# Optimization experiments

Measured on AMD Instinct MI355X. Metric: run time of the kernel, lower is better.

The kernel has to match this reference:

```python
import jax, jax.numpy as jnp
import numpy as np

EMBEDDING_DIM = 64
N_EMBEDDINGS = 512


def setup_inputs() -> dict:
    key = jax.random.key(0)
    k1, k2 = jax.random.split(key)
    inputs = jax.random.normal(k1, (32, 64, 64, 64), dtype=jnp.float32)  # NCHW, C==embedding_dim
    weight = jax.random.normal(k2, (N_EMBEDDINGS, EMBEDDING_DIM), dtype=jnp.float32)
    return {"inputs": inputs, "weight": weight}


def reference(inputs, weight):
    # NCHW -> NHWC, flatten to [N, D]
    x = jnp.transpose(inputs, (0, 2, 3, 1))  # [B, H, W, D]
    in_shape = x.shape
    flat = x.reshape(-1, EMBEDDING_DIM)  # [N, D]

    distances = (
        jnp.sum(flat * flat, axis=1, keepdims=True)
        + jnp.sum(weight * weight, axis=1)
        - 2.0 * flat @ weight.T
    )
    idx = jnp.argmin(distances, axis=1)  # [N]

    # one-hot @ weight is just a gather
    quantized = weight[idx].reshape(in_shape)  # [B, H, W, D]

    # commitment loss: mse(stop_grad(quantized), x)
    e_latent_loss = jnp.mean(jnp.square(jax.lax.stop_gradient(quantized) - x))

    # straight-through estimator
    quantized = x + jax.lax.stop_gradient(quantized - x)

    return jnp.transpose(quantized, (0, 3, 1, 2)), e_latent_loss
```

## Files before the change

kernel.cpp:

```cpp
#include <hip/hip_runtime.h>
#include <math.h>

typedef short bf16x8 __attribute__((ext_vector_type(8)));
typedef float f32x4 __attribute__((ext_vector_type(4)));

#define VQ_D 64
#define VQ_K 512
#define VQ_NQ 131072
#define VQ_TOTAL 8388608
#define QB 128
#define NT 32
#define XPITCH 136

__device__ __forceinline__ ushort bf16_rne(float f) {
    uint u = __builtin_bit_cast(uint, f);
    u += 0x7fffu + ((u >> 16) & 1u);
    return (ushort)(u >> 16);
}
__device__ __forceinline__ float bf16_to_f(ushort h) {
    uint u = ((uint)h) << 16;
    return __builtin_bit_cast(float, u);
}

__global__ __launch_bounds__(64) void vq_prep(const float* __restrict__ w,
                                              ushort* __restrict__ wfrag,
                                              float* __restrict__ wn) {
    const int k = blockIdx.x * 64 + threadIdx.x;
    const float4* row = (const float4*)(w + k * VQ_D);
    const int t = k >> 4, col = k & 15;
    double sd = 0.0;
    for (int g = 0; g < 8; ++g) {
        float4 a = row[2 * g], b4 = row[2 * g + 1];
        float v[8] = {a.x, a.y, a.z, a.w, b4.x, b4.y, b4.z, b4.w};
        ushort hi[8], lo[8];
#pragma unroll
        for (int j = 0; j < 8; ++j) {
            sd = fma((double)v[j], (double)v[j], sd);
            hi[j] = bf16_rne(v[j]);
            lo[j] = bf16_rne(v[j] - bf16_to_f(hi[j]));
        }
        const int quad = g & 3, fh = g >> 2;
        const int lane = quad * 16 + col;
        bf16x8* basez = (bf16x8*)wfrag + t * 256 + lane;
        *(basez + (fh)*64)     = *(bf16x8*)hi;
        *(basez + (2 + fh)*64) = *(bf16x8*)lo;
    }
    wn[k] = (float)sd;
}

__global__ __launch_bounds__(256, 3) void vq_main(const float* __restrict__ in,
                                                  const float* __restrict__ w,
                                                  const ushort* __restrict__ wfrag,
                                                  const float* __restrict__ wng,
                                                  float* __restrict__ out) {
    __shared__ ushort x_lds[QB * XPITCH];
    __shared__ float wn_lds[VQ_K];
    __shared__ float xn_lds[2][QB];
    __shared__ float best_lds[QB], sec_lds[QB];
    __shared__ int   bi_lds[QB], si_lds[QB];

    const int tid  = threadIdx.x;
    const int lane = tid & 63;
    const int wid  = tid >> 6;
    const int col  = lane & 15;
    const int quad = lane >> 4;
    const int n0  = blockIdx.x * QB;
    const int b   = n0 >> 12;
    const int hw0 = n0 & 4095;
    const float* xg = in + (b << 18) + hw0;

    wn_lds[tid] = wng[tid];
    wn_lds[tid + 256] = wng[tid + 256];
    {
        const int q = tid & 127, gh = tid >> 7;
        const float* xq = xg + q;
        float xnp = 0.f;
#pragma unroll
        for (int i = 0; i < 4; ++i) {
            const int g = gh * 4 + i;
            float v[8];
            ushort hi[8], lo[8];
#pragma unroll
            for (int j = 0; j < 8; ++j) v[j] = xq[(g * 8 + j) << 12];
#pragma unroll
            for (int j = 0; j < 8; ++j) {
                xnp = fmaf(v[j], v[j], xnp);
                hi[j] = bf16_rne(v[j]);
                lo[j] = bf16_rne(v[j] - bf16_to_f(hi[j]));
            }
            *(bf16x8*)&x_lds[q * XPITCH + g * 8]      = *(bf16x8*)hi;
            *(bf16x8*)&x_lds[q * XPITCH + 64 + g * 8] = *(bf16x8*)lo;
        }
        xn_lds[gh][q] = xnp;
    }
    __syncthreads();

    const int arow0 = wid * 32 + col;
    bf16x8 ah0[2], ah1[2], al0[2], al1[2];
#pragma unroll
    for (int T = 0; T < 2; ++T) {
        const ushort* xr = x_lds + (arow0 + T * 16) * XPITCH;
        ah0[T] = *(const bf16x8*)(xr + quad * 8);
        ah1[T] = *(const bf16x8*)(xr + 32 + quad * 8);
        al0[T] = *(const bf16x8*)(xr + 64 + quad * 8);
        al1[T] = *(const bf16x8*)(xr + 96 + quad * 8);
    }

    float best[8], secnd[8];
    int bI[8], sI[8];
#pragma unroll
    for (int r = 0; r < 8; ++r) { best[r] = 3.4e38f; secnd[r] = 3.4e38f; bI[r] = 0; sI[r] = 0; }

    const bf16x8* wf = (const bf16x8*)wfrag + lane;
    bf16x8 bh0 = wf[0], bh1 = wf[64], bl0 = wf[128], bl1 = wf[192];

    for (int t = 0; t < NT; ++t) {
        bf16x8 nh0, nh1, nl0, nl1;
        if (t + 1 < NT) {
            const bf16x8* nx = wf + (t + 1) * 256;
            nh0 = nx[0]; nh1 = nx[64]; nl0 = nx[128]; nl1 = nx[192];
        }
        const float wnv = wn_lds[t * 16 + col];
#pragma unroll
        for (int T = 0; T < 2; ++T) {
            f32x4 accP = {0.f, 0.f, 0.f, 0.f}, accQ = {0.f, 0.f, 0.f, 0.f};
            accP = __builtin_amdgcn_mfma_f32_16x16x32_bf16(ah0[T], bh0, accP, 0, 0, 0);
            accP = __builtin_amdgcn_mfma_f32_16x16x32_bf16(ah1[T], bh1, accP, 0, 0, 0);
            accQ = __builtin_amdgcn_mfma_f32_16x16x32_bf16(ah0[T], bl0, accQ, 0, 0, 0);
            accQ = __builtin_amdgcn_mfma_f32_16x16x32_bf16(ah1[T], bl1, accQ, 0, 0, 0);
            accQ = __builtin_amdgcn_mfma_f32_16x16x32_bf16(al0[T], bh0, accQ, 0, 0, 0);
            accQ = __builtin_amdgcn_mfma_f32_16x16x32_bf16(al1[T], bh1, accQ, 0, 0, 0);
            const int kg = t * 16 + col;
#pragma unroll
            for (int j = 0; j < 4; ++j) {
                float dist = fmaf(-2.f, accP[j] + accQ[j], wnv);
                const int r = T * 4 + j;
                bool lt  = dist < best[r];
                bool lt2 = (!lt) && (dist < secnd[r]);
                secnd[r] = lt ? best[r] : (lt2 ? dist : secnd[r]);
                sI[r]    = lt ? bI[r]   : (lt2 ? kg   : sI[r]);
                best[r]  = lt ? dist    : best[r];
                bI[r]    = lt ? kg      : bI[r];
            }
        }
        bh0 = nh0; bh1 = nh1; bl0 = nl0; bl1 = nl1;
    }

#pragma unroll
    for (int off = 1; off < 16; off <<= 1) {
#pragma unroll
        for (int r = 0; r < 8; ++r) {
            float ob = __shfl_xor(best[r], off, 64);
            float os = __shfl_xor(secnd[r], off, 64);
            int   oi = __shfl_xor(bI[r], off, 64);
            int   oc = __shfl_xor(sI[r], off, 64);
            bool oWins = (ob < best[r]) || (ob == best[r] && oi < bI[r]);
            float nb  = oWins ? ob      : best[r];
            int   ni  = oWins ? oi      : bI[r];
            float c1  = oWins ? best[r] : ob;
            int   ci1 = oWins ? bI[r]   : oi;
            float c2  = oWins ? os      : secnd[r];
            int   ci2 = oWins ? oc      : sI[r];
            bool c1w = (c1 < c2) || (c1 == c2 && ci1 < ci2);
            secnd[r] = c1w ? c1 : c2;
            sI[r]    = c1w ? ci1 : ci2;
            best[r] = nb; bI[r] = ni;
        }
    }
    if (col == 0) {
#pragma unroll
        for (int r = 0; r < 8; ++r) {
            const int q = wid * 32 + (r >> 2) * 16 + quad * 4 + (r & 3);
            best_lds[q] = best[r]; sec_lds[q] = secnd[r];
            bi_lds[q] = bI[r];     si_lds[q] = sI[r];
        }
    }
    __syncthreads();

    if (tid < QB) {
        const int q = tid;
        float cb = best_lds[q], cs = sec_lds[q];
        int cbi = bi_lds[q], csi = si_lds[q];
        double chosen = (double)cb;
        if (cs - cb < 8e-3f) {
            const float* wb  = w + cbi * VQ_D;
            const float* ws2 = w + csi * VQ_D;
            const float* xqp = xg + q;
            double nb = 0.0, dotb = 0.0, ns = 0.0, dots = 0.0;
            for (int d = 0; d < VQ_D; ++d) {
                double xv = (double)xqp[d << 12];
                double wbv = (double)wb[d], wsv = (double)ws2[d];
                nb = fma(wbv, wbv, nb); dotb = fma(xv, wbv, dotb);
                ns = fma(wsv, wsv, ns); dots = fma(xv, wsv, dots);
            }
            double db = nb - 2.0 * dotb, ds = ns - 2.0 * dots;
            if (ds < db || (ds == db && csi < cbi)) { cbi = csi; chosen = ds; }
            else                                    { chosen = db; }
        }
        bi_lds[q] = cbi;
        double lq = (double)(xn_lds[0][q] + xn_lds[1][q]) + chosen;
#pragma unroll
        for (int off = 32; off > 0; off >>= 1)
            lq += __shfl_down(lq, off, 64);
        if ((tid & 63) == 0)
            atomicAdd(out + VQ_TOTAL, (float)(lq * (1.0 / (double)VQ_TOTAL)));
    }
    __syncthreads();

    {
        const int q = tid & 127, half = tid >> 7;
        const float4* wrow = (const float4*)(w + bi_lds[q] * VQ_D) + half * 8;
        float* op = out + (b << 18) + hw0 + q;
#pragma unroll
        for (int u = 0; u < 8; ++u) {
            float4 v = wrow[u];
            const int d = half * 32 + 4 * u;
            op[(d + 0) << 12] = v.x;
            op[(d + 1) << 12] = v.y;
            op[(d + 2) << 12] = v.z;
            op[(d + 3) << 12] = v.w;
        }
    }
}

extern "C" void kernel_launch(void* const* d_in, const int* in_sizes, int n_in,
                              void* d_out, int out_size, void* d_ws, size_t ws_size,
                              hipStream_t stream) {
    const float* in = (const float*)d_in[0];
    const float* w  = (const float*)d_in[1];
    float* out = (float*)d_out;

    ushort* wfrag = (ushort*)d_ws;
    float*  wn    = (float*)((char*)d_ws + 131072);

    hipMemsetAsync(out + VQ_TOTAL, 0, sizeof(float), stream);
    vq_prep<<<8, 64, 0, stream>>>(w, wfrag, wn);
    vq_main<<<VQ_NQ / QB, 256, 0, stream>>>(in, w, wfrag, wn, out);
}
```

Measured before the change: 141.0 us.

## Double queries per block and pack codebook tile index into distance low bits

Each block now handles 256 queries instead of 128, so every wave runs four 16-row MFMA tiles per codebook fragment load and the weight-fragment traffic per query is halved. The x tile is staged into LDS in two passes to keep the LDS footprint unchanged. The top-2 tracking in the inner loop packs the tile index into the low 5 mantissa bits of the distance, replacing compare-and-select chains with fmin/fmax. The memset is folded into the prep kernel, which also drops its double-precision norm accumulation. Register pressure rises (occupancy hint lowered from 3 to 2), and the bit packing slightly perturbs the distances, which the existing fp64 near-tie recheck is meant to absorb.

```diff
diff --git a/kernel.cpp b/kernel.cpp
--- a/kernel.cpp
+++ b/kernel.cpp
@@ -8,7 +8,7 @@
 #define VQ_K 512
 #define VQ_NQ 131072
 #define VQ_TOTAL 8388608
-#define QB 128
+#define QB 256
 #define NT 32
 #define XPITCH 136
 
@@ -22,38 +22,40 @@
     return __builtin_bit_cast(float, u);
 }
 
-__global__ __launch_bounds__(64) void vq_prep(const float* __restrict__ w,
-                                              ushort* __restrict__ wfrag,
-                                              float* __restrict__ wn) {
-    const int k = blockIdx.x * 64 + threadIdx.x;
+__global__ __launch_bounds__(128) void vq_prep(const float* __restrict__ w,
+                                               ushort* __restrict__ wfrag,
+                                               float* __restrict__ wn,
+                                               float* __restrict__ out) {
+    if (blockIdx.x == 0 && threadIdx.x == 0) out[VQ_TOTAL] = 0.f;
+    const int k = blockIdx.x * 128 + threadIdx.x;
     const float4* row = (const float4*)(w + k * VQ_D);
     const int t = k >> 4, col = k & 15;
-    double sd = 0.0;
+    float nrm = 0.f;
     for (int g = 0; g < 8; ++g) {
         float4 a = row[2 * g], b4 = row[2 * g + 1];
         float v[8] = {a.x, a.y, a.z, a.w, b4.x, b4.y, b4.z, b4.w};
         ushort hi[8], lo[8];
 #pragma unroll
         for (int j = 0; j < 8; ++j) {
-            sd = fma((double)v[j], (double)v[j], sd);
+            nrm = fmaf(v[j], v[j], nrm);
             hi[j] = bf16_rne(v[j]);
             lo[j] = bf16_rne(v[j] - bf16_to_f(hi[j]));
         }
         const int quad = g & 3, fh = g >> 2;
         const int lane = quad * 16 + col;
         bf16x8* basez = (bf16x8*)wfrag + t * 256 + lane;
-        *(basez + (fh)*64)     = *(bf16x8*)hi;
-        *(basez + (2 + fh)*64) = *(bf16x8*)lo;
-    }
-    wn[k] = (float)sd;
-}
-
-__global__ __launch_bounds__(256, 3) void vq_main(const float* __restrict__ in,
+        *(basez + fh * 64)       = *(bf16x8*)hi;
+        *(basez + (2 + fh) * 64) = *(bf16x8*)lo;
+    }
+    wn[k] = nrm;
+}
+
+__global__ __launch_bounds__(256, 2) void vq_main(const float* __restrict__ in,
                                                   const float* __restrict__ w,
                                                   const ushort* __restrict__ wfrag,
                                                   const float* __restrict__ wng,
                                                   float* __restrict__ out) {
-    __shared__ ushort x_lds[QB * XPITCH];
+    __shared__ ushort x_lds[128 * XPITCH];
     __shared__ float wn_lds[VQ_K];
     __shared__ float xn_lds[2][QB];
     __shared__ float best_lds[QB], sec_lds[QB];
@@ -69,47 +71,53 @@
     const int hw0 = n0 & 4095;
     const float* xg = in + (b << 18) + hw0;
 
-    wn_lds[tid] = wng[tid];
+    wn_lds[tid]       = wng[tid];
     wn_lds[tid + 256] = wng[tid + 256];
-    {
-        const int q = tid & 127, gh = tid >> 7;
-        const float* xq = xg + q;
-        float xnp = 0.f;
-#pragma unroll
-        for (int i = 0; i < 4; ++i) {
-            const int g = gh * 4 + i;
-            float v[8];
-            ushort hi[8], lo[8];
-#pragma unroll
-            for (int j = 0; j < 8; ++j) v[j] = xq[(g * 8 + j) << 12];
-#pragma unroll
-            for (int j = 0; j < 8; ++j) {
-                xnp = fmaf(v[j], v[j], xnp);
-                hi[j] = bf16_rne(v[j]);
-                lo[j] = bf16_rne(v[j] - bf16_to_f(hi[j]));
-            }
-            *(bf16x8*)&x_lds[q * XPITCH + g * 8]      = *(bf16x8*)hi;
-            *(bf16x8*)&x_lds[q * XPITCH + 64 + g * 8] = *(bf16x8*)lo;
-        }
-        xn_lds[gh][q] = xnp;
-    }
-    __syncthreads();
-
-    const int arow0 = wid * 32 + col;
-    bf16x8 ah0[2], ah1[2], al0[2], al1[2];
-#pragma unroll
-    for (int T = 0; T < 2; ++T) {
-        const ushort* xr = x_lds + (arow0 + T * 16) * XPITCH;
-        ah0[T] = *(const bf16x8*)(xr + quad * 8);
-        ah1[T] = *(const bf16x8*)(xr + 32 + quad * 8);
-        al0[T] = *(const bf16x8*)(xr + 64 + quad * 8);
-        al1[T] = *(const bf16x8*)(xr + 96 + quad * 8);
-    }
-
-    float best[8], secnd[8];
-    int bI[8], sI[8];
-#pragma unroll
-    for (int r = 0; r < 8; ++r) { best[r] = 3.4e38f; secnd[r] = 3.4e38f; bI[r] = 0; sI[r] = 0; }
+
+    bf16x8 ah0[4], ah1[4], al0[4], al1[4];
+    const int q_l = tid & 127, gh = tid >> 7;
+    const int arow_l = (wid & 1) * 64 + col;
+
+#pragma unroll
+    for (int p = 0; p < 2; ++p) {
+        {
+            const float* xq = xg + p * 128 + q_l;
+            float xnp = 0.f;
+#pragma unroll
+            for (int i = 0; i < 4; ++i) {
+                const int g = gh * 4 + i;
+                float v[8];
+                ushort hi[8], lo[8];
+#pragma unroll
+                for (int j = 0; j < 8; ++j) v[j] = xq[(g * 8 + j) << 12];
+#pragma unroll
+                for (int j = 0; j < 8; ++j) {
+                    xnp = fmaf(v[j], v[j], xnp);
+                    hi[j] = bf16_rne(v[j]);
+                    lo[j] = bf16_rne(v[j] - bf16_to_f(hi[j]));
+                }
+                *(bf16x8*)&x_lds[q_l * XPITCH + g * 8]      = *(bf16x8*)hi;
+                *(bf16x8*)&x_lds[q_l * XPITCH + 64 + g * 8] = *(bf16x8*)lo;
+            }
+            xn_lds[gh][p * 128 + q_l] = xnp;
+        }
+        __syncthreads();
+        if ((wid >> 1) == p) {
+#pragma unroll
+            for (int T = 0; T < 4; ++T) {
+                const ushort* xr = x_lds + (arow_l + T * 16) * XPITCH;
+                ah0[T] = *(const bf16x8*)(xr + quad * 8);
+                ah1[T] = *(const bf16x8*)(xr + 32 + quad * 8);
+                al0[T] = *(const bf16x8*)(xr + 64 + quad * 8);
+                al1[T] = *(const bf16x8*)(xr + 96 + quad * 8);
+            }
+        }
+        __syncthreads();
+    }
+
+    float best[16], secnd[16];
+#pragma unroll
+    for (int r = 0; r < 16; ++r) { best[r] = 3.0e38f; secnd[r] = 3.0e38f; }
 
     const bf16x8* wf = (const bf16x8*)wfrag + lane;
     bf16x8 bh0 = wf[0], bh1 = wf[64], bl0 = wf[128], bl1 = wf[192];
@@ -122,7 +130,7 @@
         }
         const float wnv = wn_lds[t * 16 + col];
 #pragma unroll
-        for (int T = 0; T < 2; ++T) {
+        for (int T = 0; T < 4; ++T) {
             f32x4 accP = {0.f, 0.f, 0.f, 0.f}, accQ = {0.f, 0.f, 0.f, 0.f};
             accP = __builtin_amdgcn_mfma_f32_16x16x32_bf16(ah0[T], bh0, accP, 0, 0, 0);
             accP = __builtin_amdgcn_mfma_f32_16x16x32_bf16(ah1[T], bh1, accP, 0, 0, 0);
@@ -130,54 +138,64 @@
             accQ = __builtin_amdgcn_mfma_f32_16x16x32_bf16(ah1[T], bl1, accQ, 0, 0, 0);
             accQ = __builtin_amdgcn_mfma_f32_16x16x32_bf16(al0[T], bh0, accQ, 0, 0, 0);
             accQ = __builtin_amdgcn_mfma_f32_16x16x32_bf16(al1[T], bh1, accQ, 0, 0, 0);
-            const int kg = t * 16 + col;
 #pragma unroll
             for (int j = 0; j < 4; ++j) {
                 float dist = fmaf(-2.f, accP[j] + accQ[j], wnv);
+                uint u = (__builtin_bit_cast(uint, dist) & 0xFFFFFFE0u) | (uint)t;
+                float key = __builtin_bit_cast(float, u);
                 const int r = T * 4 + j;
-                bool lt  = dist < best[r];
-                bool lt2 = (!lt) && (dist < secnd[r]);
-                secnd[r] = lt ? best[r] : (lt2 ? dist : secnd[r]);
-                sI[r]    = lt ? bI[r]   : (lt2 ? kg   : sI[r]);
-                best[r]  = lt ? dist    : best[r];
-                bI[r]    = lt ? kg      : bI[r];
+                float m = fmaxf(best[r], key);
+                best[r]  = fminf(best[r], key);
+                secnd[r] = fminf(secnd[r], m);
             }
         }
         bh0 = nh0; bh1 = nh1; bl0 = nl0; bl1 = nl1;
     }
 
+    float bD[16], sD[16];
+    int bI[16], sI[16];
+#pragma unroll
+    for (int r = 0; r < 16; ++r) {
+        uint ub = __builtin_bit_cast(uint, best[r]);
+        uint us = __builtin_bit_cast(uint, secnd[r]);
+        bI[r] = (int)(ub & 31u) * 16 + col;
+        sI[r] = (int)(us & 31u) * 16 + col;
+        bD[r] = __builtin_bit_cast(float, ub & 0xFFFFFFE0u);
+        sD[r] = __builtin_bit_cast(float, us & 0xFFFFFFE0u);
+    }
+
 #pragma unroll
     for (int off = 1; off < 16; off <<= 1) {
 #pragma unroll
-        for (int r = 0; r < 8; ++r) {
-            float ob = __shfl_xor(best[r], off, 64);
-            float os = __shfl_xor(secnd[r], off, 64);
+        for (int r = 0; r < 16; ++r) {
+            float ob = __shfl_xor(bD[r], off, 64);
+            float os = __shfl_xor(sD[r], off, 64);
             int   oi = __shfl_xor(bI[r], off, 64);
             int   oc = __shfl_xor(sI[r], off, 64);
-            bool oWins = (ob < best[r]) || (ob == best[r] && oi < bI[r]);
-            float nb  = oWins ? ob      : best[r];
-            int   ni  = oWins ? oi      : bI[r];
-            float c1  = oWins ? best[r] : ob;
-            int   ci1 = oWins ? bI[r]   : oi;
-            float c2  = oWins ? os      : secnd[r];
-            int   ci2 = oWins ? oc      : sI[r];
+            bool oWins = (ob < bD[r]) || (ob == bD[r] && oi < bI[r]);
+            float nb  = oWins ? ob    : bD[r];
+            int   ni  = oWins ? oi    : bI[r];
+            float c1  = oWins ? bD[r] : ob;
+            int   ci1 = oWins ? bI[r] : oi;
+            float c2  = oWins ? os    : sD[r];
+            int   ci2 = oWins ? oc    : sI[r];
             bool c1w = (c1 < c2) || (c1 == c2 && ci1 < ci2);
-            secnd[r] = c1w ? c1 : c2;
-            sI[r]    = c1w ? ci1 : ci2;
-            best[r] = nb; bI[r] = ni;
+            sD[r] = c1w ? c1  : c2;
+            sI[r] = c1w ? ci1 : ci2;
+            bD[r] = nb; bI[r] = ni;
         }
     }
     if (col == 0) {
 #pragma unroll
-        for (int r = 0; r < 8; ++r) {
-            const int q = wid * 32 + (r >> 2) * 16 + quad * 4 + (r & 3);
-            best_lds[q] = best[r]; sec_lds[q] = secnd[r];
-            bi_lds[q] = bI[r];     si_lds[q] = sI[r];
+        for (int r = 0; r < 16; ++r) {
+            const int q = wid * 64 + (r >> 2) * 16 + quad * 4 + (r & 3);
+            best_lds[q] = bD[r]; sec_lds[q] = sD[r];
+            bi_lds[q] = bI[r];   si_lds[q] = sI[r];
         }
     }
     __syncthreads();
 
-    if (tid < QB) {
+    {
         const int q = tid;
         float cb = best_lds[q], cs = sec_lds[q];
         int cbi = bi_lds[q], csi = si_lds[q];
@@ -208,17 +226,16 @@
     __syncthreads();
 
     {
-        const int q = tid & 127, half = tid >> 7;
-        const float4* wrow = (const float4*)(w + bi_lds[q] * VQ_D) + half * 8;
+        const int q = tid;
+        const float4* wrow = (const float4*)(w + bi_lds[q] * VQ_D);
         float* op = out + (b << 18) + hw0 + q;
 #pragma unroll
-        for (int u = 0; u < 8; ++u) {
-            float4 v = wrow[u];
-            const int d = half * 32 + 4 * u;
-            op[(d + 0) << 12] = v.x;
-            op[(d + 1) << 12] = v.y;
-            op[(d + 2) << 12] = v.z;
-            op[(d + 3) << 12] = v.w;
+        for (int i = 0; i < 16; ++i) {
+            float4 v = wrow[i];
+            op[(4 * i + 0) << 12] = v.x;
+            op[(4 * i + 1) << 12] = v.y;
+            op[(4 * i + 2) << 12] = v.z;
+            op[(4 * i + 3) << 12] = v.w;
         }
     }
 }
@@ -233,7 +250,6 @@
     ushort* wfrag = (ushort*)d_ws;
     float*  wn    = (float*)((char*)d_ws + 131072);
 
-    hipMemsetAsync(out + VQ_TOTAL, 0, sizeof(float), stream);
-    vq_prep<<<8, 64, 0, stream>>>(w, wfrag, wn);
+    vq_prep<<<4, 128, 0, stream>>>(w, wfrag, wn, out);
     vq_main<<<VQ_NQ / QB, 256, 0, stream>>>(in, w, wfrag, wn, out);
 }
```

After: 141.9 us. About the same (+0.6%).
